# Performance work log

Measured on AMD Instinct MI355X. Metric: run time of the kernel, lower is better.

Reference implementation:

```python
import jax, jax.numpy as jnp
import numpy as np

H = 512  # hidden/input size
T = 16384
CLAMP_MAX = 49688.0

def setup_inputs() -> dict:
    key = jax.random.key(0)
    ks = jax.random.split(key, 12)
    s = 0.05
    x = jax.random.normal(ks[0], (T, 1, H), dtype=jnp.float32)
    W_ih = jax.random.normal(ks[1], (4 * H, H), dtype=jnp.float32) * s
    W_hh = jax.random.normal(ks[2], (4 * H, H), dtype=jnp.float32) * s
    b_ih = jax.random.normal(ks[3], (4 * H,), dtype=jnp.float32) * s
    b_hh = jax.random.normal(ks[4], (4 * H,), dtype=jnp.float32) * s
    fc_w = jax.random.normal(ks[5], (128, H), dtype=jnp.float32) * s
    fc_b = jax.random.normal(ks[6], (128,), dtype=jnp.float32) * s
    fc1_w = jax.random.normal(ks[7], (16, 128), dtype=jnp.float32) * s
    fc1_b = jax.random.normal(ks[8], (16,), dtype=jnp.float32) * s
    fc2_w = jax.random.normal(ks[9], (37, 128), dtype=jnp.float32) * s
    fc2_b = jax.random.normal(ks[10], (37,), dtype=jnp.float32) * s
    return {"x": x, "W_ih": W_ih, "W_hh": W_hh, "b_ih": b_ih, "b_hh": b_hh,
            "fc_w": fc_w, "fc_b": fc_b, "fc1_w": fc1_w, "fc1_b": fc1_b,
            "fc2_w": fc2_w, "fc2_b": fc2_b}

def _lstm(x, W_ih, W_hh, b_ih, b_hh):
    # x: [T, 1, H] seq-major, batch=1. Precompute input contribution for all t.
    xf = x.reshape(-1, H)                       # [T, H]
    x_gates = xf @ W_ih.T + (b_ih + b_hh)       # [T, 4H]

    def step(carry, xg):
        h, c = carry                            # [H], [H]
        g = xg + W_hh @ h                       # [4H]
        i = jax.nn.sigmoid(g[:H])
        f = jax.nn.sigmoid(g[H:2 * H])
        gg = jnp.tanh(g[2 * H:3 * H])
        o = jax.nn.sigmoid(g[3 * H:])
        c = f * c + i * gg
        h = o * jnp.tanh(c)
        return (h, c), h

    h0 = jnp.zeros((H,), dtype=x.dtype)
    c0 = jnp.zeros((H,), dtype=x.dtype)
    _, hs = jax.lax.scan(step, (h0, c0), x_gates)  # hs: [T, H]
    return hs

def reference(x, W_ih, W_hh, b_ih, b_hh, fc_w, fc_b, fc1_w, fc1_b, fc2_w, fc2_b):
    hs = _lstm(x, W_ih, W_hh, b_ih, b_hh)       # [T, H]
    inter = hs @ fc_w.T + fc_b                  # [T, 128]
    action = jnp.clip(inter @ fc1_w.T + fc1_b, 0.0, CLAMP_MAX)  # [T, 16]
    obj = jnp.clip(inter @ fc2_w.T + fc2_b, 0.0, CLAMP_MAX)     # [T, 37]
    return (action, obj)
```

## Files before the change

### kernel.cpp

```cpp
#include <hip/hip_runtime.h>
#include <hip/hip_bf16.h>
#include <stdint.h>

#define T_LEN 16384
#define HDIM 512
#define G4 2048
#define CLAMP_MAXV 49688.0f

#define XG_OFF    0ull
#define HS_OFF    134217728ull
#define INTER_OFF 167772160ull
#define HREC_OFF  176160768ull
#define BSUM_OFF  176168960ull
#define WS_NEED   176177152ull

__global__ __launch_bounds__(256) void init_k(uint64_t* __restrict__ hrec,
                                              const float* __restrict__ b_ih,
                                              const float* __restrict__ b_hh,
                                              float* __restrict__ bsum) {
    int i = blockIdx.x * 256 + threadIdx.x;
    if (i < 1024) hrec[i] = 0ull;
    bsum[i] = b_ih[i] + b_hh[i];
}

__global__ __launch_bounds__(256) void gemm_abt(const float* __restrict__ A,
                                                const float* __restrict__ B,
                                                const float* __restrict__ bias,
                                                float* __restrict__ C,
                                                int N, int K) {
    __shared__ float As[16][68];
    __shared__ float Bs[16][68];
    const int tid = threadIdx.x;
    const int bm = blockIdx.x << 6, bn = blockIdx.y << 6;
    const int tx = tid & 15, ty = tid >> 4;
    const int lr = tid >> 2, lk = (tid & 3) << 2;
    float acc[4][4] = {};
    const float* Ap = A + (size_t)(bm + lr) * K + lk;
    const float* Bp = B + (size_t)(bn + lr) * K + lk;
    for (int kt = 0; kt < K; kt += 16) {
        float4 av = *(const float4*)(Ap + kt);
        float4 bv = *(const float4*)(Bp + kt);
        __syncthreads();
        As[lk + 0][lr] = av.x; As[lk + 1][lr] = av.y;
        As[lk + 2][lr] = av.z; As[lk + 3][lr] = av.w;
        Bs[lk + 0][lr] = bv.x; Bs[lk + 1][lr] = bv.y;
        Bs[lk + 2][lr] = bv.z; Bs[lk + 3][lr] = bv.w;
        __syncthreads();
#pragma unroll
        for (int kk = 0; kk < 16; ++kk) {
            float4 a4 = *(const float4*)&As[kk][ty << 2];
            float4 b4 = *(const float4*)&Bs[kk][tx << 2];
            acc[0][0] += a4.x * b4.x; acc[0][1] += a4.x * b4.y;
            acc[0][2] += a4.x * b4.z; acc[0][3] += a4.x * b4.w;
            acc[1][0] += a4.y * b4.x; acc[1][1] += a4.y * b4.y;
            acc[1][2] += a4.y * b4.z; acc[1][3] += a4.y * b4.w;
            acc[2][0] += a4.z * b4.x; acc[2][1] += a4.z * b4.y;
            acc[2][2] += a4.z * b4.z; acc[2][3] += a4.z * b4.w;
            acc[3][0] += a4.w * b4.x; acc[3][1] += a4.w * b4.y;
            acc[3][2] += a4.w * b4.z; acc[3][3] += a4.w * b4.w;
        }
    }
    const int col = bn + (tx << 2);
    float4 bv4 = *(const float4*)&bias[col];
#pragma unroll
    for (int i = 0; i < 4; ++i) {
        int row = bm + (ty << 2) + i;
        float4 o;
        o.x = acc[i][0] + bv4.x; o.y = acc[i][1] + bv4.y;
        o.z = acc[i][2] + bv4.z; o.w = acc[i][3] + bv4.w;
        *(float4*)&C[(size_t)row * N + col] = o;
    }
}

__global__ __launch_bounds__(512, 2) void lstm_scan(const float* __restrict__ W_hh,
                                                    const float* __restrict__ xg,
                                                    float* __restrict__ hs,
                                                    uint64_t* __restrict__ hrec) {
    __shared__ float h_lds[512];
    __shared__ float part[512];
    const int tid = threadIdx.x;
    const int wv = tid >> 6;
    const int lane = tid & 63;
    const int j = blockIdx.x;
    const int rowg = ((lane >> 4) << 9) | (j << 4) | (lane & 15);

    float4 w4[16];
    {
        const float4* wp = (const float4*)(W_hh + (size_t)rowg * HDIM + (wv << 6));
#pragma unroll
        for (int q = 0; q < 16; ++q) w4[q] = wp[q];
    }

    float c_reg = 0.f;
    for (int t = 0; t < T_LEN; ++t) {
        float xgv = 0.f;
        if (wv == 0) xgv = xg[(size_t)t * G4 + rowg];

        uint64_t* src = hrec + ((t & 1) << 9) + tid;
        uint64_t u;
        int guard = 0;
        do {
            u = __hip_atomic_load(src, __ATOMIC_RELAXED, __HIP_MEMORY_SCOPE_AGENT);
        } while ((uint32_t)(u >> 32) != (uint32_t)t && ++guard < (1 << 18));
        h_lds[tid] = __uint_as_float((uint32_t)u);
        __syncthreads();

        float ac0 = 0.f, ac1 = 0.f, ac2 = 0.f, ac3 = 0.f;
        const float* hp = h_lds + (wv << 6);
#pragma unroll
        for (int q = 0; q < 16; q += 4) {
            float4 h0 = *(const float4*)(hp + (q << 2));
            float4 h1 = *(const float4*)(hp + ((q + 1) << 2));
            float4 h2 = *(const float4*)(hp + ((q + 2) << 2));
            float4 h3 = *(const float4*)(hp + ((q + 3) << 2));
            ac0 += w4[q].x * h0.x + w4[q].y * h0.y + w4[q].z * h0.z + w4[q].w * h0.w;
            ac1 += w4[q + 1].x * h1.x + w4[q + 1].y * h1.y + w4[q + 1].z * h1.z + w4[q + 1].w * h1.w;
            ac2 += w4[q + 2].x * h2.x + w4[q + 2].y * h2.y + w4[q + 2].z * h2.z + w4[q + 2].w * h2.w;
            ac3 += w4[q + 3].x * h3.x + w4[q + 3].y * h3.y + w4[q + 3].z * h3.z + w4[q + 3].w * h3.w;
        }
        part[tid] = (ac0 + ac1) + (ac2 + ac3);
        __syncthreads();

        if (wv == 0) {
            float g = xgv;
#pragma unroll
            for (int ww = 0; ww < 8; ++ww) g += part[(ww << 6) | lane];
            bool isg = (lane >= 32) && (lane < 48);
            float y = isg ? (g + g) : g;
            float s = 1.f / (1.f + __expf(-y));
            float a = isg ? (s + s - 1.f) : s;
            float fa = __shfl_down(a, 16);
            float ga = __shfl_down(a, 32);
            float oa = __shfl_down(a, 48);
            if (lane < 16) {
                c_reg = fa * c_reg + a * ga;
                float e2 = __expf(-2.f * c_reg);
                float hv = oa * (2.f / (1.f + e2) - 1.f);
                hs[(size_t)t * HDIM + (j << 4) + lane] = hv;
                uint64_t pu = ((uint64_t)(uint32_t)(t + 1) << 32) |
                              (uint64_t)__float_as_uint(hv);
                __hip_atomic_store(hrec + (((t + 1) & 1) << 9) + (j << 4) + lane, pu,
                                   __ATOMIC_RELAXED, __HIP_MEMORY_SCOPE_AGENT);
            }
        }
    }
}

__global__ __launch_bounds__(256) void heads_k(const float* __restrict__ inter,
                                               const float* __restrict__ fc1w,
                                               const float* __restrict__ fc1b,
                                               const float* __restrict__ fc2w,
                                               const float* __restrict__ fc2b,
                                               float* __restrict__ out) {
    __shared__ float it[64][128];
    __shared__ float wt[128][56];
    __shared__ float bl[56];
    const int tid = threadIdx.x;
    const int t0 = blockIdx.x << 6;
    for (int q = tid; q < 64 * 32; q += 256) {
        int r = q >> 5, c4 = q & 31;
        *(float4*)&it[r][c4 << 2] =
            *(const float4*)&inter[(size_t)(t0 + r) * 128 + (c4 << 2)];
    }
    for (int q = tid; q < 53 * 32; q += 256) {
        int r = q >> 5, c4 = q & 31;
        float4 v = (r < 16) ? ((const float4*)&fc1w[r * 128])[c4]
                            : ((const float4*)&fc2w[(r - 16) * 128])[c4];
        int k = c4 << 2;
        wt[k + 0][r] = v.x; wt[k + 1][r] = v.y; wt[k + 2][r] = v.z; wt[k + 3][r] = v.w;
    }
    if (tid < 53) bl[tid] = (tid < 16) ? fc1b[tid] : fc2b[tid - 16];
    __syncthreads();
    const int c = tid & 63, rg = tid >> 6;
    if (c < 53) {
        float b = bl[c];
        for (int rr = 0; rr < 16; ++rr) {
            int r = (rg << 4) + rr;
            float acc = b;
#pragma unroll 8
            for (int k = 0; k < 128; k += 4) {
                float4 iv = *(const float4*)&it[r][k];
                acc += iv.x * wt[k][c] + iv.y * wt[k + 1][c] +
                       iv.z * wt[k + 2][c] + iv.w * wt[k + 3][c];
            }
            acc = fminf(fmaxf(acc, 0.f), CLAMP_MAXV);
            int t = t0 + r;
            if (c < 16) out[(size_t)t * 16 + c] = acc;
            else        out[262144 + (size_t)t * 37 + (c - 16)] = acc;
        }
    }
}

extern "C" void kernel_launch(void* const* d_in, const int* in_sizes, int n_in,
                              void* d_out, int out_size, void* d_ws, size_t ws_size,
                              hipStream_t stream) {
    const float* x     = (const float*)d_in[0];
    const float* W_ih  = (const float*)d_in[1];
    const float* W_hh  = (const float*)d_in[2];
    const float* b_ih  = (const float*)d_in[3];
    const float* b_hh  = (const float*)d_in[4];
    const float* fc_w  = (const float*)d_in[5];
    const float* fc_b  = (const float*)d_in[6];
    const float* fc1_w = (const float*)d_in[7];
    const float* fc1_b = (const float*)d_in[8];
    const float* fc2_w = (const float*)d_in[9];
    const float* fc2_b = (const float*)d_in[10];

    if (ws_size < WS_NEED) return;

    char* ws = (char*)d_ws;
    float*    xg    = (float*)(ws + XG_OFF);
    float*    hs    = (float*)(ws + HS_OFF);
    float*    inter = (float*)(ws + INTER_OFF);
    uint64_t* hrec  = (uint64_t*)(ws + HREC_OFF);
    float*    bsum  = (float*)(ws + BSUM_OFF);
    float*    out   = (float*)d_out;

    hipLaunchKernelGGL(init_k, dim3(8), dim3(256), 0, stream, hrec, b_ih, b_hh, bsum);
    hipLaunchKernelGGL(gemm_abt, dim3(256, 32), dim3(256), 0, stream,
                       x, W_ih, bsum, xg, 2048, 512);
    hipLaunchKernelGGL(lstm_scan, dim3(32), dim3(512), 0, stream, W_hh, xg, hs, hrec);
    hipLaunchKernelGGL(gemm_abt, dim3(256, 2), dim3(256), 0, stream,
                       hs, fc_w, fc_b, inter, 128, 512);
    hipLaunchKernelGGL(heads_k, dim3(256), dim3(256), 0, stream,
                       inter, fc1_w, fc1_b, fc2_w, fc2_b, out);
}
```

Measured before the change: 27.28 ms.

## Co-locate scan blocks on one XCD and sync via L2-local volatile flags

The grid grows to 256 blocks, but only every eighth block does work. With round-robin block placement across XCDs, the 32 active blocks should land on the same XCD and share its L2. The per-step hidden-state exchange then uses plain volatile loads and stores to a fast buffer, kept alongside agent-scope atomics to a slow buffer that any block falls back to after a bounded spin. The first __syncthreads is replaced by an LDS waitcnt, since each wave only reads the h values it wrote itself, and the partial-sum buffer is double-buffered by step parity. xg loads and hs stores become nontemporal. The change depends on an undocumented block-to-XCD placement; if the guess is wrong, blocks pay the slow fallback path instead.

```diff
diff --git a/kernel.cpp b/kernel.cpp
--- a/kernel.cpp
+++ b/kernel.cpp
@@ -10,16 +10,18 @@
 #define XG_OFF    0ull
 #define HS_OFF    134217728ull
 #define INTER_OFF 167772160ull
-#define HREC_OFF  176160768ull
-#define BSUM_OFF  176168960ull
+#define HFAST_OFF 167772160ull
+#define HSLOW_OFF 167780352ull
+#define BSUM_OFF  167788544ull
 #define WS_NEED   176177152ull
 
-__global__ __launch_bounds__(256) void init_k(uint64_t* __restrict__ hrec,
+__global__ __launch_bounds__(256) void init_k(uint64_t* __restrict__ hfast,
+                                              uint64_t* __restrict__ hslow,
                                               const float* __restrict__ b_ih,
                                               const float* __restrict__ b_hh,
                                               float* __restrict__ bsum) {
     int i = blockIdx.x * 256 + threadIdx.x;
-    if (i < 1024) hrec[i] = 0ull;
+    if (i < 1024) { hfast[i] = 0ull; hslow[i] = 0ull; }
     bsum[i] = b_ih[i] + b_hh[i];
 }
 
@@ -72,16 +74,18 @@
     }
 }
 
-__global__ __launch_bounds__(512, 2) void lstm_scan(const float* __restrict__ W_hh,
+__global__ __launch_bounds__(512, 1) void lstm_scan(const float* __restrict__ W_hh,
                                                     const float* __restrict__ xg,
                                                     float* __restrict__ hs,
-                                                    uint64_t* __restrict__ hrec) {
+                                                    uint64_t* __restrict__ hfast,
+                                                    uint64_t* __restrict__ hslow) {
+    if (blockIdx.x & 7) return;
+    const int j = blockIdx.x >> 3;
     __shared__ float h_lds[512];
-    __shared__ float part[512];
+    __shared__ float part[2][512];
     const int tid = threadIdx.x;
     const int wv = tid >> 6;
     const int lane = tid & 63;
-    const int j = blockIdx.x;
     const int rowg = ((lane >> 4) << 9) | (j << 4) | (lane & 15);
 
     float4 w4[16];
@@ -89,21 +93,42 @@
         const float4* wp = (const float4*)(W_hh + (size_t)rowg * HDIM + (wv << 6));
 #pragma unroll
         for (int q = 0; q < 16; ++q) w4[q] = wp[q];
-    }
-
+#pragma unroll
+        for (int q = 0; q < 16; ++q)
+            asm volatile("" : "+v"(w4[q].x), "+v"(w4[q].y),
+                              "+v"(w4[q].z), "+v"(w4[q].w));
+    }
+
+    int use_slow = 0;
     float c_reg = 0.f;
     for (int t = 0; t < T_LEN; ++t) {
+        const int par = t & 1;
         float xgv = 0.f;
-        if (wv == 0) xgv = xg[(size_t)t * G4 + rowg];
-
-        uint64_t* src = hrec + ((t & 1) << 9) + tid;
-        uint64_t u;
-        int guard = 0;
-        do {
-            u = __hip_atomic_load(src, __ATOMIC_RELAXED, __HIP_MEMORY_SCOPE_AGENT);
-        } while ((uint32_t)(u >> 32) != (uint32_t)t && ++guard < (1 << 18));
+        if (wv == 0) xgv = __builtin_nontemporal_load(&xg[(size_t)t * G4 + rowg]);
+
+        uint64_t u = 0;
+        {
+            const volatile uint64_t* fsrc =
+                (const volatile uint64_t*)(hfast + (par << 9) + tid);
+            if (!use_slow) {
+                int tries = 0;
+                for (;;) {
+                    u = *fsrc;
+                    if ((uint32_t)(u >> 32) == (uint32_t)t) break;
+                    if (++tries >= 4096) { use_slow = 1; break; }
+                }
+            }
+            if (use_slow) {
+                uint64_t* ssrc = hslow + (par << 9) + tid;
+                int g = 0;
+                do {
+                    u = __hip_atomic_load(ssrc, __ATOMIC_RELAXED,
+                                          __HIP_MEMORY_SCOPE_AGENT);
+                } while ((uint32_t)(u >> 32) != (uint32_t)t && ++g < (1 << 22));
+            }
+        }
         h_lds[tid] = __uint_as_float((uint32_t)u);
-        __syncthreads();
+        asm volatile("s_waitcnt lgkmcnt(0)" ::: "memory");
 
         float ac0 = 0.f, ac1 = 0.f, ac2 = 0.f, ac3 = 0.f;
         const float* hp = h_lds + (wv << 6);
@@ -118,13 +143,13 @@
             ac2 += w4[q + 2].x * h2.x + w4[q + 2].y * h2.y + w4[q + 2].z * h2.z + w4[q + 2].w * h2.w;
             ac3 += w4[q + 3].x * h3.x + w4[q + 3].y * h3.y + w4[q + 3].z * h3.z + w4[q + 3].w * h3.w;
         }
-        part[tid] = (ac0 + ac1) + (ac2 + ac3);
+        part[par][tid] = (ac0 + ac1) + (ac2 + ac3);
         __syncthreads();
 
         if (wv == 0) {
             float g = xgv;
 #pragma unroll
-            for (int ww = 0; ww < 8; ++ww) g += part[(ww << 6) | lane];
+            for (int ww = 0; ww < 8; ++ww) g += part[par][(ww << 6) | lane];
             bool isg = (lane >= 32) && (lane < 48);
             float y = isg ? (g + g) : g;
             float s = 1.f / (1.f + __expf(-y));
@@ -136,11 +161,13 @@
                 c_reg = fa * c_reg + a * ga;
                 float e2 = __expf(-2.f * c_reg);
                 float hv = oa * (2.f / (1.f + e2) - 1.f);
-                hs[(size_t)t * HDIM + (j << 4) + lane] = hv;
+                __builtin_nontemporal_store(hv, &hs[(size_t)t * HDIM + (j << 4) + lane]);
                 uint64_t pu = ((uint64_t)(uint32_t)(t + 1) << 32) |
                               (uint64_t)__float_as_uint(hv);
-                __hip_atomic_store(hrec + (((t + 1) & 1) << 9) + (j << 4) + lane, pu,
-                                   __ATOMIC_RELAXED, __HIP_MEMORY_SCOPE_AGENT);
+                const int dst = (((t + 1) & 1) << 9) + (j << 4) + lane;
+                *(volatile uint64_t*)(hfast + dst) = pu;
+                __hip_atomic_store(hslow + dst, pu, __ATOMIC_RELAXED,
+                                   __HIP_MEMORY_SCOPE_AGENT);
             }
         }
     }
@@ -212,14 +239,17 @@
     float*    xg    = (float*)(ws + XG_OFF);
     float*    hs    = (float*)(ws + HS_OFF);
     float*    inter = (float*)(ws + INTER_OFF);
-    uint64_t* hrec  = (uint64_t*)(ws + HREC_OFF);
+    uint64_t* hfast = (uint64_t*)(ws + HFAST_OFF);
+    uint64_t* hslow = (uint64_t*)(ws + HSLOW_OFF);
     float*    bsum  = (float*)(ws + BSUM_OFF);
     float*    out   = (float*)d_out;
 
-    hipLaunchKernelGGL(init_k, dim3(8), dim3(256), 0, stream, hrec, b_ih, b_hh, bsum);
+    hipLaunchKernelGGL(init_k, dim3(8), dim3(256), 0, stream,
+                       hfast, hslow, b_ih, b_hh, bsum);
     hipLaunchKernelGGL(gemm_abt, dim3(256, 32), dim3(256), 0, stream,
                        x, W_ih, bsum, xg, 2048, 512);
-    hipLaunchKernelGGL(lstm_scan, dim3(32), dim3(512), 0, stream, W_hh, xg, hs, hrec);
+    hipLaunchKernelGGL(lstm_scan, dim3(256), dim3(512), 0, stream,
+                       W_hh, xg, hs, hfast, hslow);
     hipLaunchKernelGGL(gemm_abt, dim3(256, 2), dim3(256), 0, stream,
                        hs, fc_w, fc_b, inter, 128, 512);
     hipLaunchKernelGGL(heads_k, dim3(256), dim3(256), 0, stream,
```

Result: slower. 28.26 ms (+3.6%).

## Restructure LSTM scan: per-wave hidden units, wave shuffles, no block barriers

Applied to the files above, without the earlier changes.

Each wave now owns two hidden units and keeps all four gate rows for them in registers. Every lane polls the full h vector directly from global memory using cache-bypassing loads, reduces dot products with cross-lane shuffles, and computes the gates without LDS or __syncthreads. The next step's x-gate values are prefetched, and the h flag buffer is moved to overlap the inter region, which is only written after the scan. The aim is to cut the per-step barrier and LDS latency on the serial recurrence, at the cost of more global polling traffic and many more shuffle reductions per step.

```diff
diff --git a/kernel.cpp b/kernel.cpp
--- a/kernel.cpp
+++ b/kernel.cpp
@@ -7,19 +7,22 @@
 #define G4 2048
 #define CLAMP_MAXV 49688.0f
 
+typedef float f32x4 __attribute__((ext_vector_type(4)));
+typedef unsigned int u32x4 __attribute__((ext_vector_type(4)));
+
 #define XG_OFF    0ull
 #define HS_OFF    134217728ull
 #define INTER_OFF 167772160ull
-#define HREC_OFF  176160768ull
-#define BSUM_OFF  176168960ull
+#define HFAST_OFF 167772160ull
+#define BSUM_OFF  167780352ull
 #define WS_NEED   176177152ull
 
-__global__ __launch_bounds__(256) void init_k(uint64_t* __restrict__ hrec,
+__global__ __launch_bounds__(256) void init_k(uint64_t* __restrict__ hfast,
                                               const float* __restrict__ b_ih,
                                               const float* __restrict__ b_hh,
                                               float* __restrict__ bsum) {
     int i = blockIdx.x * 256 + threadIdx.x;
-    if (i < 1024) hrec[i] = 0ull;
+    if (i < 1024) hfast[i] = 0ull;
     bsum[i] = b_ih[i] + b_hh[i];
 }
 
@@ -72,77 +75,114 @@
     }
 }
 
-__global__ __launch_bounds__(512, 2) void lstm_scan(const float* __restrict__ W_hh,
+__global__ __launch_bounds__(512, 1) void lstm_scan(const float* __restrict__ W_hh,
                                                     const float* __restrict__ xg,
                                                     float* __restrict__ hs,
-                                                    uint64_t* __restrict__ hrec) {
-    __shared__ float h_lds[512];
-    __shared__ float part[512];
+                                                    uint64_t* __restrict__ hfast) {
     const int tid = threadIdx.x;
     const int wv = tid >> 6;
     const int lane = tid & 63;
     const int j = blockIdx.x;
-    const int rowg = ((lane >> 4) << 9) | (j << 4) | (lane & 15);
-
-    float4 w4[16];
-    {
-        const float4* wp = (const float4*)(W_hh + (size_t)rowg * HDIM + (wv << 6));
-#pragma unroll
-        for (int q = 0; q < 16; ++q) w4[q] = wp[q];
-    }
-
-    float c_reg = 0.f;
+    const int e0 = (j << 4) + (wv << 1);
+
+    f32x4 w[16];
+#pragma unroll
+    for (int r = 0; r < 8; ++r) {
+        const float* wr = W_hh + (size_t)(((r >> 1) << 9) + e0 + (r & 1)) * HDIM
+                        + (lane << 3);
+        asm volatile("global_load_dwordx4 %0, %2, off\n\t"
+                     "global_load_dwordx4 %1, %2, off offset:16\n\t"
+                     "s_waitcnt vmcnt(0)"
+                     : "=v"(w[2 * r]), "=v"(w[2 * r + 1]) : "v"(wr));
+    }
+
+    const int wvu = __builtin_amdgcn_readfirstlane(wv);
+    const float* xbase = xg + (j << 4) + (wvu << 1);
+    float2 xc[4], xn[4];
+#pragma unroll
+    for (int g = 0; g < 4; ++g) xc[g] = *(const float2*)(xbase + (g << 9));
+
+    const unsigned int* pb0 = (const unsigned int*)hfast + (lane << 4);
+    const unsigned int* pb1 = (const unsigned int*)(hfast + 512) + (lane << 4);
+
+    float c0 = 0.f, c1 = 0.f;
     for (int t = 0; t < T_LEN; ++t) {
-        float xgv = 0.f;
-        if (wv == 0) xgv = xg[(size_t)t * G4 + rowg];
-
-        uint64_t* src = hrec + ((t & 1) << 9) + tid;
-        uint64_t u;
-        int guard = 0;
-        do {
-            u = __hip_atomic_load(src, __ATOMIC_RELAXED, __HIP_MEMORY_SCOPE_AGENT);
-        } while ((uint32_t)(u >> 32) != (uint32_t)t && ++guard < (1 << 18));
-        h_lds[tid] = __uint_as_float((uint32_t)u);
-        __syncthreads();
-
-        float ac0 = 0.f, ac1 = 0.f, ac2 = 0.f, ac3 = 0.f;
-        const float* hp = h_lds + (wv << 6);
-#pragma unroll
-        for (int q = 0; q < 16; q += 4) {
-            float4 h0 = *(const float4*)(hp + (q << 2));
-            float4 h1 = *(const float4*)(hp + ((q + 1) << 2));
-            float4 h2 = *(const float4*)(hp + ((q + 2) << 2));
-            float4 h3 = *(const float4*)(hp + ((q + 3) << 2));
-            ac0 += w4[q].x * h0.x + w4[q].y * h0.y + w4[q].z * h0.z + w4[q].w * h0.w;
-            ac1 += w4[q + 1].x * h1.x + w4[q + 1].y * h1.y + w4[q + 1].z * h1.z + w4[q + 1].w * h1.w;
-            ac2 += w4[q + 2].x * h2.x + w4[q + 2].y * h2.y + w4[q + 2].z * h2.z + w4[q + 2].w * h2.w;
-            ac3 += w4[q + 3].x * h3.x + w4[q + 3].y * h3.y + w4[q + 3].z * h3.z + w4[q + 3].w * h3.w;
-        }
-        part[tid] = (ac0 + ac1) + (ac2 + ac3);
-        __syncthreads();
-
-        if (wv == 0) {
-            float g = xgv;
-#pragma unroll
-            for (int ww = 0; ww < 8; ++ww) g += part[(ww << 6) | lane];
-            bool isg = (lane >= 32) && (lane < 48);
-            float y = isg ? (g + g) : g;
-            float s = 1.f / (1.f + __expf(-y));
-            float a = isg ? (s + s - 1.f) : s;
-            float fa = __shfl_down(a, 16);
-            float ga = __shfl_down(a, 32);
-            float oa = __shfl_down(a, 48);
-            if (lane < 16) {
-                c_reg = fa * c_reg + a * ga;
-                float e2 = __expf(-2.f * c_reg);
-                float hv = oa * (2.f / (1.f + e2) - 1.f);
-                hs[(size_t)t * HDIM + (j << 4) + lane] = hv;
-                uint64_t pu = ((uint64_t)(uint32_t)(t + 1) << 32) |
-                              (uint64_t)__float_as_uint(hv);
-                __hip_atomic_store(hrec + (((t + 1) & 1) << 9) + (j << 4) + lane, pu,
-                                   __ATOMIC_RELAXED, __HIP_MEMORY_SCOPE_AGENT);
-            }
-        }
+        const unsigned int* pb = (t & 1) ? pb1 : pb0;
+        u32x4 q0, q1, q2, q3;
+        const unsigned int tt = (unsigned int)t;
+        int rounds = 0;
+        for (;;) {
+            asm volatile(
+                "global_load_dwordx4 %0, %4, off sc0 sc1\n\t"
+                "global_load_dwordx4 %1, %4, off offset:16 sc0 sc1\n\t"
+                "global_load_dwordx4 %2, %4, off offset:32 sc0 sc1\n\t"
+                "global_load_dwordx4 %3, %4, off offset:48 sc0 sc1\n\t"
+                "s_waitcnt vmcnt(0)"
+                : "=v"(q0), "=v"(q1), "=v"(q2), "=v"(q3)
+                : "v"(pb) : "memory");
+            if ((q0.y == tt) & (q0.w == tt) & (q1.y == tt) & (q1.w == tt) &
+                (q2.y == tt) & (q2.w == tt) & (q3.y == tt) & (q3.w == tt)) break;
+            if (++rounds > (1 << 20)) break;
+        }
+
+        if (t + 1 < T_LEN) {
+            const float* xp = xbase + (size_t)(t + 1) * G4;
+#pragma unroll
+            for (int g = 0; g < 4; ++g) xn[g] = *(const float2*)(xp + (g << 9));
+        }
+
+        const float h0 = __uint_as_float(q0.x), h1 = __uint_as_float(q0.z);
+        const float h2 = __uint_as_float(q1.x), h3 = __uint_as_float(q1.z);
+        const float h4 = __uint_as_float(q2.x), h5 = __uint_as_float(q2.z);
+        const float h6 = __uint_as_float(q3.x), h7 = __uint_as_float(q3.z);
+        float p[8];
+#pragma unroll
+        for (int r = 0; r < 8; ++r) {
+            p[r] = w[2 * r][0] * h0 + w[2 * r][1] * h1
+                 + w[2 * r][2] * h2 + w[2 * r][3] * h3
+                 + w[2 * r + 1][0] * h4 + w[2 * r + 1][1] * h5
+                 + w[2 * r + 1][2] * h6 + w[2 * r + 1][3] * h7;
+        }
+
+#pragma unroll
+        for (int s = 1; s < 64; s <<= 1) {
+#pragma unroll
+            for (int r = 0; r < 8; ++r) p[r] += __shfl_xor(p[r], s);
+        }
+
+#pragma unroll
+        for (int r = 0; r < 8; ++r)
+            p[r] += (r & 1) ? xc[r >> 1].y : xc[r >> 1].x;
+
+        float hv0, hv1;
+        {
+            float i0 = 1.f / (1.f + __expf(-p[0]));
+            float f0 = 1.f / (1.f + __expf(-p[2]));
+            float g0 = 2.f / (1.f + __expf(-2.f * p[4])) - 1.f;
+            float o0 = 1.f / (1.f + __expf(-p[6]));
+            c0 = f0 * c0 + i0 * g0;
+            hv0 = o0 * (2.f / (1.f + __expf(-2.f * c0)) - 1.f);
+            float i1 = 1.f / (1.f + __expf(-p[1]));
+            float f1 = 1.f / (1.f + __expf(-p[3]));
+            float g1 = 2.f / (1.f + __expf(-2.f * p[5])) - 1.f;
+            float o1 = 1.f / (1.f + __expf(-p[7]));
+            c1 = f1 * c1 + i1 * g1;
+            hv1 = o1 * (2.f / (1.f + __expf(-2.f * c1)) - 1.f);
+        }
+
+        if (lane == 0) {
+            float2 hw; hw.x = hv0; hw.y = hv1;
+            *(float2*)&hs[(size_t)t * HDIM + e0] = hw;
+            u32x4 pk;
+            pk.x = __float_as_uint(hv0); pk.y = (unsigned int)(t + 1);
+            pk.z = __float_as_uint(hv1); pk.w = (unsigned int)(t + 1);
+            const uint64_t* dst = hfast + (((t + 1) & 1) << 9) + e0;
+            asm volatile("global_store_dwordx4 %0, %1, off sc0 sc1"
+                         :: "v"(dst), "v"(pk) : "memory");
+        }
+
+#pragma unroll
+        for (int g = 0; g < 4; ++g) xc[g] = xn[g];
     }
 }
 
@@ -212,14 +252,16 @@
     float*    xg    = (float*)(ws + XG_OFF);
     float*    hs    = (float*)(ws + HS_OFF);
     float*    inter = (float*)(ws + INTER_OFF);
-    uint64_t* hrec  = (uint64_t*)(ws + HREC_OFF);
+    uint64_t* hfast = (uint64_t*)(ws + HFAST_OFF);
     float*    bsum  = (float*)(ws + BSUM_OFF);
     float*    out   = (float*)d_out;
 
-    hipLaunchKernelGGL(init_k, dim3(8), dim3(256), 0, stream, hrec, b_ih, b_hh, bsum);
+    hipLaunchKernelGGL(init_k, dim3(8), dim3(256), 0, stream,
+                       hfast, b_ih, b_hh, bsum);
     hipLaunchKernelGGL(gemm_abt, dim3(256, 32), dim3(256), 0, stream,
                        x, W_ih, bsum, xg, 2048, 512);
-    hipLaunchKernelGGL(lstm_scan, dim3(32), dim3(512), 0, stream, W_hh, xg, hs, hrec);
+    hipLaunchKernelGGL(lstm_scan, dim3(32), dim3(512), 0, stream,
+                       W_hh, xg, hs, hfast);
     hipLaunchKernelGGL(gemm_abt, dim3(256, 2), dim3(256), 0, stream,
                        hs, fc_w, fc_b, inter, 128, 512);
     hipLaunchKernelGGL(heads_k, dim3(256), dim3(256), 0, stream,
```

After: 96.79 ms. 3.55x slower.
